# Kernel optimization log

Hardware: AMD Instinct MI355X
Metric: run time of the kernel (lower is better)

## Reference

```python
import jax, jax.numpy as jnp
import numpy as np

B, T, D_MODEL, H, W = 2, 3, 32, 256, 256
N_HEADS, N_LEVELS, N_POINTS = 4, 3, 4


def conv2d(x, w, b, padding=1, dilation=1):
    y = jax.lax.conv_general_dilated(
        x, w, window_strides=(1, 1),
        padding=[(padding, padding), (padding, padding)],
        rhs_dilation=(dilation, dilation),
        dimension_numbers=('NCHW', 'OIHW', 'NCHW'))
    return y + b[None, :, None, None]


def lrelu(x):
    return jnp.where(x >= 0, x, 0.1 * x)


def bilinear_sample(img, x, y):
    # img: (N,C,H,W); x,y: (N,H',W') pixel coords; zero padding outside (grid_sample zeros)
    N, C, Hh, Ww = img.shape
    x0 = jnp.floor(x); y0 = jnp.floor(y)
    lx = x - x0; ly = y - y0
    imf = img.reshape(N, C, Hh * Ww)
    out = jnp.zeros((N, C) + x.shape[1:], img.dtype)
    for dy, dx, wgt in ((0, 0, (1 - lx) * (1 - ly)), (0, 1, lx * (1 - ly)),
                        (1, 0, (1 - lx) * ly), (1, 1, lx * ly)):
        xi = x0 + dx; yi = y0 + dy
        valid = (xi >= 0) & (xi < Ww) & (yi >= 0) & (yi < Hh)
        idx = (jnp.clip(yi, 0, Hh - 1) * Ww + jnp.clip(xi, 0, Ww - 1)).astype(jnp.int32)
        g = jnp.take_along_axis(imf, idx.reshape(N, 1, -1), axis=2).reshape((N, C) + x.shape[1:])
        out = out + g * (wgt * valid)[:, None]
    return out


def flow_warp(x, flow):
    # torch flow_warp with align_corners=True == sampling at pixel coords grid+flow
    N, C, Hh, Ww = x.shape
    gy, gx = jnp.meshgrid(jnp.arange(Hh, dtype=x.dtype), jnp.arange(Ww, dtype=x.dtype), indexing='ij')
    return bilinear_sample(x, gx[None] + flow[:, 0], gy[None] + flow[:, 1])


def ms_deform_attn(value, sampling_locations, attention_weights, h, w):
    # value: (N, L*h*w, Hh, d); loc: (N, Lq, Hh, L, P, 2) in [0,1]; weights: (N, Lq, Hh, L, P)
    # Matches MSDA CUDA kernel: sample at loc*(W,H)-0.5, bilinear, zero pad outside.
    N, _, Hh, d = value.shape
    Lq = sampling_locations.shape[1]
    L, P = sampling_locations.shape[3], sampling_locations.shape[4]
    out = jnp.zeros((N, Lq, Hh, d), value.dtype)
    for l in range(L):
        v = value[:, l * h * w:(l + 1) * h * w].transpose(0, 2, 1, 3)  # (N,Hh,hw,d)
        loc = sampling_locations[:, :, :, l]  # (N,Lq,Hh,P,2)
        x = loc[..., 0] * w - 0.5
        y = loc[..., 1] * h - 0.5
        x0 = jnp.floor(x); y0 = jnp.floor(y)
        lx = x - x0; ly = y - y0
        samp = jnp.zeros((N, Lq, Hh, P, d), value.dtype)
        for dy, dx, wgt in ((0, 0, (1 - lx) * (1 - ly)), (0, 1, lx * (1 - ly)),
                            (1, 0, (1 - lx) * ly), (1, 1, lx * ly)):
            xi = x0 + dx; yi = y0 + dy
            valid = (xi >= 0) & (xi < w) & (yi >= 0) & (yi < h)
            idx = (jnp.clip(yi, 0, h - 1) * w + jnp.clip(xi, 0, w - 1)).astype(jnp.int32)
            idx = idx.transpose(0, 2, 1, 3).reshape(N, Hh, Lq * P)
            g = jnp.take_along_axis(v, idx[..., None], axis=2)  # (N,Hh,Lq*P,d)
            g = g.reshape(N, Hh, Lq, P, d).transpose(0, 2, 1, 3, 4)
            samp = samp + g * (wgt * valid)[..., None]
        out = out + (samp * attention_weights[:, :, :, l][..., None]).sum(axis=3)
    return out.reshape(N, Lq, Hh * d)


def setup_inputs() -> dict:
    key = jax.random.key(0)
    ks = jax.random.split(key, 24)
    def rn(k, shape, s=1.0):
        return jax.random.normal(k, shape, dtype=jnp.float32) * s
    c = D_MODEL
    nofp = N_HEADS * N_LEVELS * N_POINTS
    return {
        'frame': rn(ks[0], (B, T, c, H, W)),
        'srcframe': rn(ks[1], (B, T, c, H, W)),
        'flow_forward': rn(ks[2], (B, T - 1, 2, H, W), 2.0),
        'flow_backward': rn(ks[3], (B, T - 1, 2, H, W), 2.0),
        'W_qk': rn(ks[4], (3 * c, 3 * c + 4, 3, 3), 0.05), 'b_qk': rn(ks[5], (3 * c,), 0.05),
        'W_v': rn(ks[6], (3 * c, 3 * c, 3, 3), 0.05), 'b_v': rn(ks[7], (3 * c,), 0.05),
        'W_vp': rn(ks[8], (c, c, 3, 3), 0.05), 'b_vp': rn(ks[9], (c,), 0.05),
        'W_off': rn(ks[10], (nofp * 2, 3 * c, 3, 3), 0.01), 'b_off': rn(ks[11], (nofp * 2,), 0.5),
        'W_aw': rn(ks[12], (nofp, 3 * c, 3, 3), 0.05), 'b_aw': rn(ks[13], (nofp,), 0.05),
        'W_out': rn(ks[14], (c, c, 3, 3), 0.05), 'b_out': rn(ks[15], (c,), 0.05),
        'W_ffd': rn(ks[16], (c, c, 3, 3), 0.05), 'b_ffd': rn(ks[17], (c,), 0.05),
        'W_ff1': rn(ks[18], (c, 2 * c, 3, 3), 0.05), 'b_ff1': rn(ks[19], (c,), 0.05),
        'W_ff2': rn(ks[20], (c, c, 3, 3), 0.05), 'b_ff2': rn(ks[21], (c,), 0.05),
        'W_fu': rn(ks[22], (c, c, 1, 1), 0.05), 'b_fu': rn(ks[23], (c,), 0.05),
    }


def reference(frame, srcframe, flow_forward, flow_backward,
              W_qk, b_qk, W_v, b_v, W_vp, b_vp, W_off, b_off, W_aw, b_aw,
              W_out, b_out, W_ffd, b_ffd, W_ff1, b_ff1, W_ff2, b_ff2, W_fu, b_fu):
    b, t, c, h, w = frame.shape
    Hh, L, P = N_HEADS, N_LEVELS, N_POINTS
    d = c // Hh
    # flow-warped neighbor frames + flows -> query embedding
    warp01 = flow_warp(frame[:, 0], flow_backward[:, 0])
    warp21 = flow_warp(frame[:, 2], flow_forward[:, 1])
    qk_in = jnp.concatenate([warp01, frame[:, 1], warp21,
                             flow_forward[:, 1], flow_backward[:, 0]], axis=1)
    qureys = lrelu(conv2d(qk_in, W_qk, b_qk))                       # (b, 3c, h, w)
    value = conv2d(frame.reshape(b, t * c, h, w), W_v, b_v)         # (b, 3c, h, w)
    # --- MSDeformAttn_Fusion ---
    val = conv2d(value.reshape(b * t, c, h, w), W_vp, b_vp).reshape(b, t, c, h, w)
    off = conv2d(qureys, W_off, b_off)                               # (b, Hh*L*P*2, h, w)
    aw = conv2d(qureys, W_aw, b_aw)                                  # (b, Hh*L*P, h, w)
    value_flat = val.reshape(b, t, c, h * w).transpose(0, 1, 3, 2).reshape(b, t * h * w, Hh, d)
    off = off.reshape(b, -1, h * w).transpose(0, 2, 1).reshape(b, h * w, Hh, L, P, 2)
    aw = aw.reshape(b, -1, h * w).transpose(0, 2, 1).reshape(b, h * w, Hh, L * P)
    aw = jax.nn.softmax(aw, axis=-1).reshape(b, h * w, Hh, L, P)
    # reference points: pixel centers normalized (masks all zero -> valid_ratios == 1)
    gy, gx = jnp.meshgrid((jnp.arange(h, dtype=off.dtype) + 0.5) / h,
                          (jnp.arange(w, dtype=off.dtype) + 0.5) / w, indexing='ij')
    ref = jnp.stack([gx.reshape(-1), gy.reshape(-1)], -1)            # (hw, 2) (x, y)
    normalizer = jnp.array([w, h], dtype=off.dtype)                  # same for all levels
    loc = ref[None, :, None, None, None, :] + off / normalizer
    attn_out = ms_deform_attn(value_flat, loc, aw, h, w)             # (b, hw, c)
    out = attn_out.reshape(b, h, w, c).transpose(0, 3, 1, 2)
    out = conv2d(out, W_out, b_out)                                  # output_proj
    # --- post-attention ---
    out = conv2d(out, W_ffd, b_ffd) + frame[:, 1]
    tseq = jnp.concatenate([out, srcframe[:, 1]], axis=1)            # (b, 2c, h, w)
    ff = conv2d(lrelu(conv2d(tseq, W_ff1, b_ff1, padding=2, dilation=2)), W_ff2, b_ff2)
    out = out + ff
    out = lrelu(conv2d(out, W_fu, b_fu, padding=0))                  # fusion 1x1
    return out
```

## Files before the change

### kernel.cpp

```cpp
#include <hip/hip_runtime.h>
#include <hip/hip_bf16.h>

typedef __hip_bfloat16 bf16;
typedef unsigned short us;
typedef unsigned int u32;
typedef __attribute__((ext_vector_type(8))) short short8;
typedef __attribute__((ext_vector_type(8))) unsigned short ushortx8;
typedef __attribute__((ext_vector_type(2))) float f32x2;
typedef __attribute__((ext_vector_type(4))) float f32x4;
typedef __attribute__((ext_vector_type(16))) float f32x16;

#define HW 65536
#define IMW 256
#define IMH 256

static __device__ __forceinline__ float u2f(us u) {
  return __uint_as_float(((unsigned)u) << 16);
}
static __device__ __forceinline__ us f2bu(float x) {
  bf16 h = __float2bfloat16(x);
  return *reinterpret_cast<us*>(&h);
}
static __device__ __forceinline__ unsigned pk2(float a, float b) {
  return (unsigned)f2bu(a) | ((unsigned)f2bu(b) << 16);
}

static __device__ __forceinline__ void gload_lds16(const void* g, void* l) {
  __builtin_amdgcn_global_load_lds(
      (const __attribute__((address_space(1))) u32*)g,
      (__attribute__((address_space(3))) u32*)l, 16, 0, 0);
}

struct PrepArgs {
  const float* src[9];
  us* dst[9];
  int OC[9], CIN[9], KPAD[9], LAY[9], KCH[9];
};

__global__ __launch_bounds__(256) void prep_weights(PrepArgs a) {
  int j = blockIdx.y;
  int n = blockIdx.x * 256 + threadIdx.x;
  int OC = a.OC[j], CIN = a.CIN[j], KPAD = a.KPAD[j];
  int tot = 9 * OC * KPAD;
  if (n >= tot) return;
  int oc, k;
  if (a.LAY[j] == 0) {
    int G = OC >> 4, NKC = KPAD >> 5;
    int e = n & 7;
    int m = (n >> 3) & 15;
    int q = (n >> 7) & 3;
    int rest = n >> 9;
    int kc = rest % NKC;
    int tg = rest / NKC;
    int g = tg % G;
    int t = tg / G;
    oc = g * 16 + m;
    k = kc * 32 + q * 8 + e;
    float v = (k < CIN) ? a.src[j][(size_t)(oc * CIN + k) * 9 + t] : 0.f;
    a.dst[j][n] = f2bu(v);
  } else {
    int OCT = OC >> 5;
    int KCH = a.KCH[j];
    int KHH = KCH >> 4;
    int e = n & 7;
    int l = (n >> 3) & 63;
    int rest = n >> 9;
    int jt = rest % OCT;
    int u = rest / OCT;
    int khi = u % KHH;
    int sg = u / KHH;
    int kc = sg / 9;
    oc = jt * 32 + (l & 31);
    k = kc * KCH + khi * 16 + (l >> 5) * 8 + e;
    int t = sg - kc * 9;
    float v = (k < CIN) ? a.src[j][(size_t)(oc * CIN + k) * 9 + t] : 0.f;
    a.dst[j][n] = f2bu(v);
  }
}

__global__ __launch_bounds__(256) void frame_to_nhwc(const float* __restrict__ frame,
                                                     unsigned* __restrict__ fn) {
  int pix = blockIdx.x * 256 + threadIdx.x;
  int b = blockIdx.y;
  const float* s = frame + (size_t)b * 96 * HW + pix;
  unsigned u[48];
#pragma unroll
  for (int j = 0; j < 48; ++j)
    u[j] = pk2(s[(size_t)(2 * j) * HW], s[(size_t)(2 * j + 1) * HW]);
  unsigned* d = fn + ((size_t)b * HW + pix) * 48;
#pragma unroll
  for (int j = 0; j < 12; ++j) {
    uint4 w;
    w.x = u[4 * j]; w.y = u[4 * j + 1]; w.z = u[4 * j + 2]; w.w = u[4 * j + 3];
    *(uint4*)&d[4 * j] = w;
  }
}

static __device__ void warp_nhwc(const us* __restrict__ fn, size_t bbase, int coff,
                                 float x, float y, unsigned* uo) {
  float x0f = floorf(x), y0f = floorf(y);
  float lx = x - x0f, ly = y - y0f;
  int x0 = (int)x0f, y0 = (int)y0f;
  float wt[4] = {(1.f - lx) * (1.f - ly), lx * (1.f - ly), (1.f - lx) * ly, lx * ly};
  float acc[32] = {};
#pragma unroll
  for (int k = 0; k < 4; ++k) {
    int xi = x0 + (k & 1), yi = y0 + (k >> 1);
    if ((unsigned)xi < IMW && (unsigned)yi < IMH) {
      const ushortx8* s =
          (const ushortx8*)(fn + (bbase + (size_t)yi * IMW + xi) * 96 + coff);
      float w = wt[k];
#pragma unroll
      for (int cj = 0; cj < 4; ++cj) {
        ushortx8 vv = s[cj];
#pragma unroll
        for (int e = 0; e < 8; ++e)
          acc[cj * 8 + e] = fmaf(w, u2f(vv[e]), acc[cj * 8 + e]);
      }
    }
  }
#pragma unroll
  for (int j = 0; j < 16; ++j) uo[j] = pk2(acc[2 * j], acc[2 * j + 1]);
}

__global__ __launch_bounds__(256) void build_qkin(
    const us* __restrict__ fn, const float* __restrict__ flowf,
    const float* __restrict__ flowb, unsigned* __restrict__ qk) {
  int pix = blockIdx.x * 256 + threadIdx.x;
  int b = blockIdx.y;
  int px = pix & 255, py = pix >> 8;

  float fbx = flowb[((size_t)(b * 2 + 0) * 2 + 0) * HW + pix];
  float fby = flowb[((size_t)(b * 2 + 0) * 2 + 1) * HW + pix];
  float ffx = flowf[((size_t)(b * 2 + 1) * 2 + 0) * HW + pix];
  float ffy = flowf[((size_t)(b * 2 + 1) * 2 + 1) * HW + pix];

  unsigned u[50];
  {
    const unsigned* s = (const unsigned*)(fn + ((size_t)b * HW + pix) * 96);
#pragma unroll
    for (int j = 0; j < 16; ++j) u[16 + j] = s[16 + j];
  }
  u[48] = pk2(ffx, ffy);
  u[49] = pk2(fbx, fby);

  warp_nhwc(fn, (size_t)b * HW, 0, (float)px + fbx, (float)py + fby, &u[0]);
  warp_nhwc(fn, (size_t)b * HW, 64, (float)px + ffx, (float)py + ffy, &u[32]);

  unsigned* qb = qk + ((size_t)b * HW + pix) * 50;
#pragma unroll
  for (int j = 0; j < 25; ++j) {
    uint2 t;
    t.x = u[2 * j];
    t.y = u[2 * j + 1];
    *(uint2*)(qb + 2 * j) = t;
  }
}

template <int CIN, int CST, int KPAD, int KCH, int OCT, bool LRELU>
__global__ __launch_bounds__(256) void conv3x3_m32(
    const us* __restrict__ in, const us* __restrict__ W2,
    const float* __restrict__ bias, us* __restrict__ out, int out_cst,
    int out_coff) {
  constexpr int COLS = 34, ROWS = 10, HALO = COLS * ROWS;
  constexpr int CIPAD = KCH + 8;
  constexpr int CHc = KCH / 8;
  constexpr int KHH = KCH / 16;
  constexpr int NCH = KPAD / KCH;
  constexpr int NSTG = NCH * 9;
  constexpr int CHB = KHH * OCT;
  __shared__ alignas(16) short lds[HALO * CIPAD];
  __shared__ alignas(16) short wlds[2][CHB * 512];

  const int z = blockIdx.z;
  const int px0 = blockIdx.x * 32, py0 = blockIdx.y * 8;
  const int lane = threadIdx.x & 63;
  const int wv = threadIdx.x >> 6;
  const int n = lane & 31;
  const int sr = n >> 4;
  const int colp = n & 15;
  const int kq = lane >> 5;

  f32x16 acc[2][OCT];
#pragma unroll
  for (int f = 0; f < 2; ++f)
#pragma unroll
    for (int j = 0; j < OCT; ++j) acc[f][j] = 0.f;

  const int rb = 2 * wv + sr;
  const int base0 = ((rb + 1) * COLS + colp + 1) * CIPAD + kq * 8;
  const int base1 = base0 + 16 * CIPAD;

  int buf = 0, sg = 0;
#pragma unroll 1
  for (int kc = 0; kc < NCH; ++kc) {
    for (int c = threadIdx.x; c < HALO * CHc; c += 256) {
      int p = c / CHc, cb = c - p * CHc;
      int row = p / COLS, col = p - row * COLS;
      int gy = py0 + row - 1, gx = px0 + col - 1;
      bool ok = ((unsigned)gy < IMH) && ((unsigned)gx < IMW);
      int cil = cb * 8;
      int cig = kc * KCH + cil;
      const us* gp = in + ((size_t)z * HW + (size_t)gy * IMW + gx) * CST + cig;
      if (CIN == KPAD) {
        short8 v = (short8)0;
        if (ok) v = *(const short8*)gp;
        *(short8*)&lds[p * CIPAD + cil] = v;
      } else {
        uint2 h0; h0.x = 0; h0.y = 0;
        uint2 h1; h1.x = 0; h1.y = 0;
        if (ok && cig + 4 <= CIN) h0 = *(const uint2*)gp;
        if (ok && cig + 8 <= CIN) h1 = *(const uint2*)(gp + 4);
        *(uint2*)&lds[p * CIPAD + cil] = h0;
        *(uint2*)&lds[p * CIPAD + cil + 4] = h1;
      }
    }
    if (kc == 0) {
#pragma unroll
      for (int r = 0; r < (CHB + 3) / 4; ++r) {
        int blk = r * 4 + wv;
        if (blk < CHB)
          gload_lds16(W2 + (size_t)(blk * 64 + lane) * 8, &wlds[0][blk * 512]);
      }
    }
    __syncthreads();

#pragma unroll 1
    for (int t = 0; t < 9; ++t, ++sg) {
      if (sg + 1 < NSTG) {
        const us* wn = W2 + (size_t)(sg + 1) * (CHB * 512);
#pragma unroll
        for (int r = 0; r < (CHB + 3) / 4; ++r) {
          int blk = r * 4 + wv;
          if (blk < CHB)
            gload_lds16(wn + (size_t)(blk * 64 + lane) * 8,
                        &wlds[buf ^ 1][blk * 512]);
        }
      }
      const int dy = t / 3 - 1, dx = t - (t / 3) * 3 - 1;
      const int toff = (dy * COLS + dx) * CIPAD;
#pragma unroll
      for (int khr = 0; khr < KHH; ++khr) {
        short8 bf0 = *(const short8*)&lds[base0 + toff + khr * 16];
        short8 bf1 = *(const short8*)&lds[base1 + toff + khr * 16];
#pragma unroll
        for (int j = 0; j < OCT; ++j) {
          short8 af =
              *(const short8*)&wlds[buf][(khr * OCT + j) * 512 + lane * 8];
          acc[0][j] = __builtin_amdgcn_mfma_f32_32x32x16_bf16(af, bf0,
                                                              acc[0][j], 0, 0, 0);
          acc[1][j] = __builtin_amdgcn_mfma_f32_32x32x16_bf16(af, bf1,
                                                              acc[1][j], 0, 0, 0);
        }
      }
      __syncthreads();
      buf ^= 1;
    }
  }

  {
    int row = py0 + rb;
#pragma unroll
    for (int f = 0; f < 2; ++f) {
      int pxc = px0 + 16 * f + colp;
      us* ob =
          out + ((size_t)z * HW + (size_t)row * IMW + pxc) * out_cst + out_coff;
#pragma unroll
      for (int j = 0; j < OCT; ++j) {
#pragma unroll
        for (int hi = 0; hi < 4; ++hi) {
          int oc0 = j * 32 + hi * 8 + kq * 4;
          f32x4 bb = *(const f32x4*)&bias[oc0];
          float v0 = acc[f][j][4 * hi + 0] + bb[0];
          float v1 = acc[f][j][4 * hi + 1] + bb[1];
          float v2 = acc[f][j][4 * hi + 2] + bb[2];
          float v3 = acc[f][j][4 * hi + 3] + bb[3];
          if (LRELU) {
            v0 = v0 >= 0.f ? v0 : 0.1f * v0;
            v1 = v1 >= 0.f ? v1 : 0.1f * v1;
            v2 = v2 >= 0.f ? v2 : 0.1f * v2;
            v3 = v3 >= 0.f ? v3 : 0.1f * v3;
          }
          uint2 w;
          w.x = pk2(v0, v1);
          w.y = pk2(v2, v3);
          *(uint2*)&ob[oc0] = w;
        }
      }
    }
  }
}

template <int CIN, int CST, int KPAD, int DIL, int G, int ZDIV, int CSUB,
          int RES, int OUTMODE, bool LRELU>
__global__ __launch_bounds__(256) void conv3x3_mfma(
    const us* __restrict__ in, const us* __restrict__ W2,
    const float* __restrict__ bias, void* __restrict__ out, int out_cst,
    int out_coff, float* __restrict__ outB, const float* __restrict__ res,
    int res_cst, int res_coff) {
  constexpr int OC = G * 16;
  constexpr int COLS = 16 + 2 * DIL;
  constexpr int ROWS = 8 + 2 * DIL;
  constexpr int HALO = ROWS * COLS;
  constexpr int CIPAD = KPAD + 8;
  constexpr int CH = KPAD / 8;
  constexpr int NKC = KPAD / 32;
  constexpr int GW0 = (G + 1) / 2;
  constexpr int NU = 9 * NKC;
  __shared__ alignas(16) short lds[HALO * CIPAD];

  const int z = blockIdx.z;
  const int bin = z / ZDIV;
  const int coff = (z % ZDIV) * CSUB;
  const int px0 = blockIdx.x * 16, py0 = blockIdx.y * 8;
  const int lane = threadIdx.x & 63;
  const int wv = threadIdx.x >> 6;
  const int m = lane & 15, q = lane >> 4;
  const int gh = wv & 1, rh = wv >> 1;
  const int goff = gh * GW0;

  f32x4 acc[GW0][4];
#pragma unroll
  for (int g = 0; g < GW0; ++g)
#pragma unroll
    for (int r = 0; r < 4; ++r) acc[g][r] = 0.f;

  for (int c = threadIdx.x; c < HALO * CH; c += 256) {
    int p = c / CH, cb = c - p * CH;
    int row = p / COLS, col = p - row * COLS;
    int gy = py0 + row - DIL, gx = px0 + col - DIL;
    bool ok = ((unsigned)gy < IMH) && ((unsigned)gx < IMW);
    int ci0 = cb * 8;
    const us* gp = in + ((size_t)bin * HW + (size_t)gy * IMW + gx) * CST + coff + ci0;
    if (CIN == KPAD) {
      short8 v = (short8)0;
      if (ok) v = *(const short8*)gp;
      *(short8*)&lds[p * CIPAD + ci0] = v;
    } else {
      uint2 h0; h0.x = 0; h0.y = 0;
      uint2 h1; h1.x = 0; h1.y = 0;
      if (ok && ci0 + 4 <= CIN) h0 = *(const uint2*)gp;
      if (ok && ci0 + 8 <= CIN) h1 = *(const uint2*)(gp + 4);
      *(uint2*)&lds[p * CIPAD + ci0] = h0;
      *(uint2*)&lds[p * CIPAD + ci0 + 4] = h1;
    }
  }
  __syncthreads();

  const us* wl = W2 + (size_t)lane * 8;
  short8 af[2][GW0];
#pragma unroll
  for (int g = 0; g < GW0; ++g)
    if (goff + g < G)
      af[0][g] = *(const short8*)(wl + (size_t)((goff + g) * NKC) * 512);

#pragma unroll
  for (int u = 0; u < NU; ++u) {
    const int t = u / NKC, kc = u - t * NKC;
    if (u + 1 < NU) {
      const int t1 = (u + 1) / NKC, kc1 = (u + 1) - t1 * NKC;
#pragma unroll
      for (int g = 0; g < GW0; ++g)
        if (goff + g < G)
          af[(u + 1) & 1][g] =
              *(const short8*)(wl + (size_t)((t1 * G + goff + g) * NKC + kc1) * 512);
    }
    const int dy = t / 3 - 1, dx = t - (t / 3) * 3 - 1;
    short8 bfr[4];
#pragma unroll
    for (int r = 0; r < 4; ++r) {
      int rr = rh * 4 + r + DIL + dy * DIL;
      int cc = m + DIL + dx * DIL;
      bfr[r] = *(const short8*)&lds[(rr * COLS + cc) * CIPAD + kc * 32 + q * 8];
    }
#pragma unroll
    for (int g = 0; g < GW0; ++g)
      if (goff + g < G)
#pragma unroll
        for (int r = 0; r < 4; ++r)
          acc[g][r] = __builtin_amdgcn_mfma_f32_16x16x32_bf16(af[u & 1][g], bfr[r],
                                                              acc[g][r], 0, 0, 0);
  }

#pragma unroll
  for (int g = 0; g < GW0; ++g) {
    if (goff + g < G) {
      int oc0 = (goff + g) * 16 + q * 4;
      f32x4 bb = *(const f32x4*)&bias[oc0];
#pragma unroll
      for (int r = 0; r < 4; ++r) {
        int py = py0 + rh * 4 + r;
        int px = px0 + m;
        size_t pix = (size_t)py * IMW + px;
        f32x4 v;
#pragma unroll
        for (int e = 0; e < 4; ++e) {
          float x = acc[g][r][e] + bb[e];
          if (LRELU) x = x >= 0.f ? x : 0.1f * x;
          v[e] = x;
        }
        if (RES == 1) {
          f32x4 rv = *(const f32x4*)&res[((size_t)z * HW + pix) * res_cst + oc0];
#pragma unroll
          for (int e = 0; e < 4; ++e) v[e] += rv[e];
        }
        if (RES == 2) {
#pragma unroll
          for (int e = 0; e < 4; ++e)
            v[e] += res[((size_t)z * res_cst + res_coff + oc0 + e) * HW + pix];
        }
        if (OUTMODE == 0 || OUTMODE == 3) {
          uint2 w;
          w.x = pk2(v[0], v[1]);
          w.y = pk2(v[2], v[3]);
          *(uint2*)&((us*)out)[((size_t)z * HW + pix) * out_cst + out_coff + oc0] = w;
        }
        if (OUTMODE == 2)
          *(f32x4*)&((float*)out)[((size_t)z * HW + pix) * out_cst + oc0] = v;
        if (OUTMODE == 3)
          *(f32x4*)&outB[((size_t)z * HW + pix) * 32 + oc0] = v;
      }
    }
  }
}

__global__ __launch_bounds__(256) void deform_attn(
    const us* __restrict__ valp, const us* __restrict__ off,
    const float* __restrict__ aw, us* __restrict__ outp) {
  int tid = threadIdx.x;
  int half = tid & 1;
  int hh = (tid >> 1) & 3;
  int pix = blockIdx.x * 32 + (tid >> 3);
  int b = blockIdx.y;
  int px = pix & (IMW - 1), py = pix >> 8;

  us os[12];
  {
    const uint2* ob = (const uint2*)(off + ((size_t)b * HW + pix) * 96 +
                                     hh * 24 + half * 12);
    uint2 a0 = ob[0], a1 = ob[1], a2 = ob[2];
    *(uint2*)&os[0] = a0;
    *(uint2*)&os[4] = a1;
    *(uint2*)&os[8] = a2;
  }
  float wv[6];
  {
    const f32x2* ab = (const f32x2*)(aw + ((size_t)b * HW + pix) * 48 +
                                     hh * 12 + half * 6);
    f32x2 a0 = ab[0], a1 = ab[1], a2 = ab[2];
    wv[0] = a0.x; wv[1] = a0.y; wv[2] = a1.x;
    wv[3] = a1.y; wv[4] = a2.x; wv[5] = a2.y;
  }

  float m6 = wv[0];
#pragma unroll
  for (int i = 1; i < 6; ++i) m6 = fmaxf(m6, wv[i]);
  float mx = fmaxf(m6, __shfl_xor(m6, 1));
  float s6 = 0.f;
#pragma unroll
  for (int i = 0; i < 6; ++i) {
    wv[i] = __expf(wv[i] - mx);
    s6 += wv[i];
  }
  float inv = 1.f / (s6 + __shfl_xor(s6, 1));

  f32x2 acc2[4];
#pragma unroll
  for (int j = 0; j < 4; ++j) acc2[j] = 0.f;

#pragma unroll
  for (int i = 0; i < 6; ++i) {
    int pp = half * 6 + i;
    int l = pp >> 2;
    const us* vbase = valp + ((size_t)(b * 3 + l) * HW) * 32 + hh * 8;
    float x = (float)px + u2f(os[2 * i]);
    float y = (float)py + u2f(os[2 * i + 1]);
    float x0f = floorf(x), y0f = floorf(y);
    float lx = x - x0f, ly = y - y0f;
    int x0 = (int)x0f, y0 = (int)y0f;
    bool vx0 = (unsigned)x0 < IMW, vx1 = (unsigned)(x0 + 1) < IMW;
    bool vy0 = (unsigned)y0 < IMH, vy1 = (unsigned)(y0 + 1) < IMH;
    float a = wv[i] * inv;
    float ax0 = (1.f - lx) * a, ax1 = lx * a;
    float w00 = ax0 * (1.f - ly), w01 = ax1 * (1.f - ly);
    float w10 = ax0 * ly, w11 = ax1 * ly;
    const us* p00 = vbase + (size_t)((long)(y0 * IMW + x0)) * 32;
#pragma unroll
    for (int c = 0; c < 4; ++c) {
      bool ok = (c & 1 ? vx1 : vx0) && (c & 2 ? vy1 : vy0);
      float w = (c == 0) ? w00 : (c == 1) ? w01 : (c == 2) ? w10 : w11;
      const us* p = p00 + (c & 1) * 32 + (c >> 1) * (IMW * 32);
      if (ok) {
        uint4 uu = *(const uint4*)p;
        unsigned uarr[4] = {uu.x, uu.y, uu.z, uu.w};
#pragma unroll
        for (int j = 0; j < 4; ++j) {
          f32x2 v;
          v.x = __uint_as_float(uarr[j] << 16);
          v.y = __uint_as_float(uarr[j] & 0xffff0000u);
          acc2[j] += v * w;
        }
      }
    }
  }

  float accf[8];
#pragma unroll
  for (int j = 0; j < 4; ++j) {
    accf[2 * j] = acc2[j].x + __shfl_xor(acc2[j].x, 1);
    accf[2 * j + 1] = acc2[j].y + __shfl_xor(acc2[j].y, 1);
  }
  if (half == 0) {
    ushortx8 sv;
#pragma unroll
    for (int dd = 0; dd < 8; ++dd) sv[dd] = f2bu(accf[dd]);
    *(ushortx8*)(outp + ((size_t)b * HW + pix) * 32 + hh * 8) = sv;
  }
}

__global__ __launch_bounds__(256) void copy_src(const float* __restrict__ src,
                                                unsigned* __restrict__ out1b) {
  int pix = blockIdx.x * 256 + threadIdx.x;
  int b = blockIdx.y;
  const float* s = src + ((size_t)(b * 3 + 1) * 32) * HW + pix;
  unsigned u[16];
#pragma unroll
  for (int j = 0; j < 16; ++j)
    u[j] = pk2(s[(size_t)(2 * j) * HW], s[(size_t)(2 * j + 1) * HW]);
  unsigned* d = out1b + ((size_t)b * HW + pix) * 32 + 16;
#pragma unroll
  for (int j = 0; j < 4; ++j) {
    uint4 w;
    w.x = u[4 * j]; w.y = u[4 * j + 1]; w.z = u[4 * j + 2]; w.w = u[4 * j + 3];
    *(uint4*)&d[4 * j] = w;
  }
}

__global__ __launch_bounds__(256) void conv1x1_fu(
    const float* __restrict__ in, const float* __restrict__ wgt,
    const float* __restrict__ bias, float* __restrict__ out) {
  int pix = blockIdx.x * 256 + threadIdx.x;
  int b = blockIdx.y;
  float vin[32];
  {
    const f32x4* s = (const f32x4*)(in + ((size_t)b * HW + pix) * 32);
#pragma unroll
    for (int j = 0; j < 8; ++j) {
      f32x4 v = s[j];
#pragma unroll
      for (int e = 0; e < 4; ++e) vin[4 * j + e] = v[e];
    }
  }
#pragma unroll 1
  for (int oc = 0; oc < 32; ++oc) {
    float a = bias[oc];
#pragma unroll
    for (int ci = 0; ci < 32; ++ci) a = fmaf(wgt[oc * 32 + ci], vin[ci], a);
    a = a >= 0.f ? a : 0.1f * a;
    out[((size_t)b * 32 + oc) * HW + pix] = a;
  }
}

extern "C" void kernel_launch(void* const* d_in, const int* in_sizes, int n_in,
                              void* d_out, int out_size, void* d_ws, size_t ws_size,
                              hipStream_t stream) {
  (void)in_sizes; (void)n_in; (void)out_size;
  if (ws_size < 25614592ull * 4) return;

  const float* frame = (const float*)d_in[0];
  const float* srcframe = (const float*)d_in[1];
  const float* flowf = (const float*)d_in[2];
  const float* flowb = (const float*)d_in[3];

  float* ws = (float*)d_ws;
  us* wsu = (us*)d_ws;

  static const int w2off[9] = {0,      110592, 193536, 202752, 285696,
                               327168, 336384, 345600, 364032};
  us* fnhwc = (us*)(ws + 186624);
  unsigned* qk_u = (unsigned*)(ws + 6478080);
  us* qk = (us*)qk_u;
  us* Q = (us*)(ws + 13031680);
  us* V = (us*)(ws + 6478080);
  us* Vp = (us*)(ws + 19323136);
  us* offb = (us*)(ws + 186624);
  float* awb = (float*)(ws + 6478080);
  us* attn = (us*)(ws + 13031680);
  us* convout = (us*)(ws + 13031680 + 2097152);
  us* out1b = (us*)(ws + 6478080);
  unsigned* out1b_u = (unsigned*)out1b;
  float* out1f = (float*)(ws + 19323136);
  us* ff1out = (us*)(ws + 186624);
  float* out2 = (float*)(ws + 13031680);

  {
    PrepArgs pa;
    static const int srcidx[9] = {4, 6, 8, 10, 12, 14, 16, 18, 20};
    static const int OCs[9] = {96, 96, 32, 96, 48, 32, 32, 32, 32};
    static const int CINs[9] = {100, 96, 32, 96, 96, 32, 32, 64, 32};
    static const int KPADs[9] = {128, 96, 32, 96, 96, 32, 32, 64, 32};
    static const int LAYs[9] = {1, 1, 0, 1, 0, 0, 0, 0, 0};
    static const int KCHs[9] = {32, 32, 32, 32, 32, 32, 32, 32, 32};
    for (int i = 0; i < 9; ++i) {
      pa.src[i] = (const float*)d_in[srcidx[i]];
      pa.dst[i] = wsu + w2off[i];
      pa.OC[i] = OCs[i];
      pa.CIN[i] = CINs[i];
      pa.KPAD[i] = KPADs[i];
      pa.LAY[i] = LAYs[i];
      pa.KCH[i] = KCHs[i];
    }
    prep_weights<<<dim3(432, 9), 256, 0, stream>>>(pa);
  }

  frame_to_nhwc<<<dim3(256, 2), 256, 0, stream>>>(frame, (unsigned*)fnhwc);

  build_qkin<<<dim3(256, 2), 256, 0, stream>>>(fnhwc, flowf, flowb, qk_u);

  dim3 cg2(16, 32, 2);
  dim3 cg32(8, 32, 2);

  conv3x3_m32<100, 100, 128, 32, 3, true><<<cg32, 256, 0, stream>>>(
      qk, wsu + w2off[0], (const float*)d_in[5], Q, 96, 0);

  conv3x3_m32<96, 96, 96, 32, 3, false><<<cg32, 256, 0, stream>>>(
      fnhwc, wsu + w2off[1], (const float*)d_in[7], V, 96, 0);

  conv3x3_mfma<32, 96, 32, 1, 2, 3, 32, 0, 0, false><<<dim3(16, 32, 6), 256, 0, stream>>>(
      V, wsu + w2off[2], (const float*)d_in[9], Vp, 32, 0, nullptr, nullptr, 0, 0);

  conv3x3_m32<96, 96, 96, 32, 3, false><<<cg32, 256, 0, stream>>>(
      Q, wsu + w2off[3], (const float*)d_in[11], offb, 96, 0);

  conv3x3_mfma<96, 96, 96, 1, 3, 1, 0, 0, 2, false><<<cg2, 256, 0, stream>>>(
      Q, wsu + w2off[4], (const float*)d_in[13], awb, 48, 0, nullptr, nullptr, 0, 0);

  deform_attn<<<dim3(2048, 2), 256, 0, stream>>>(Vp, offb, awb, attn);

  conv3x3_mfma<32, 32, 32, 1, 2, 1, 0, 0, 0, false><<<cg2, 256, 0, stream>>>(
      attn, wsu + w2off[5], (const float*)d_in[15], convout, 32, 0, nullptr, nullptr, 0, 0);

  conv3x3_mfma<32, 32, 32, 1, 2, 1, 0, 2, 3, false><<<cg2, 256, 0, stream>>>(
      convout, wsu + w2off[6], (const float*)d_in[17], out1b, 64, 0, out1f, frame, 96, 32);

  copy_src<<<dim3(256, 2), 256, 0, stream>>>(srcframe, out1b_u);

  conv3x3_mfma<64, 64, 64, 2, 2, 1, 0, 0, 0, true><<<cg2, 256, 0, stream>>>(
      out1b, wsu + w2off[7], (const float*)d_in[19], ff1out, 32, 0, nullptr, nullptr, 0, 0);

  conv3x3_mfma<32, 32, 32, 1, 2, 1, 0, 1, 2, false><<<cg2, 256, 0, stream>>>(
      ff1out, wsu + w2off[8], (const float*)d_in[21], out2, 32, 0, nullptr, out1f, 32, 0);

  conv1x1_fu<<<dim3(256, 2), 256, 0, stream>>>(out2, (const float*)d_in[22],
                                               (const float*)d_in[23], (float*)d_out);
}
```

Before: 460.5 us.

## Load conv weights directly into registers with double buffering instead of LDS

Weight fragments for each 3x3 tap are now read from global memory straight into a two-slot register array and prefetched one tap ahead. This replaces the LDS weight staging done with global_load_lds, and the tap loop is fully unrolled. The aim is to drop the per-tap __syncthreads and the LDS weight traffic. In exchange every wave loads the same weights from global/L2 on its own, and the register footprint grows, which risks occupancy loss or spills.

```diff
diff --git a/kernel.cpp b/kernel.cpp
--- a/kernel.cpp
+++ b/kernel.cpp
@@ -23,12 +23,6 @@
 }
 static __device__ __forceinline__ unsigned pk2(float a, float b) {
   return (unsigned)f2bu(a) | ((unsigned)f2bu(b) << 16);
-}
-
-static __device__ __forceinline__ void gload_lds16(const void* g, void* l) {
-  __builtin_amdgcn_global_load_lds(
-      (const __attribute__((address_space(1))) u32*)g,
-      (__attribute__((address_space(3))) u32*)l, 16, 0, 0);
 }
 
 struct PrepArgs {
@@ -167,10 +161,8 @@
   constexpr int CHc = KCH / 8;
   constexpr int KHH = KCH / 16;
   constexpr int NCH = KPAD / KCH;
-  constexpr int NSTG = NCH * 9;
-  constexpr int CHB = KHH * OCT;
+  constexpr int WST = KHH * OCT * 512;
   __shared__ alignas(16) short lds[HALO * CIPAD];
-  __shared__ alignas(16) short wlds[2][CHB * 512];
 
   const int z = blockIdx.z;
   const int px0 = blockIdx.x * 32, py0 = blockIdx.y * 8;
@@ -191,9 +183,12 @@
   const int base0 = ((rb + 1) * COLS + colp + 1) * CIPAD + kq * 8;
   const int base1 = base0 + 16 * CIPAD;
 
-  int buf = 0, sg = 0;
+  const us* wl = W2 + (size_t)lane * 8;
+  short8 af[2][KHH][OCT];
+
 #pragma unroll 1
   for (int kc = 0; kc < NCH; ++kc) {
+    if (kc) __syncthreads();
     for (int c = threadIdx.x; c < HALO * CHc; c += 256) {
       int p = c / CHc, cb = c - p * CHc;
       int row = p / COLS, col = p - row * COLS;
@@ -215,27 +210,26 @@
         *(uint2*)&lds[p * CIPAD + cil + 4] = h1;
       }
     }
-    if (kc == 0) {
-#pragma unroll
-      for (int r = 0; r < (CHB + 3) / 4; ++r) {
-        int blk = r * 4 + wv;
-        if (blk < CHB)
-          gload_lds16(W2 + (size_t)(blk * 64 + lane) * 8, &wlds[0][blk * 512]);
-      }
+    {
+      const us* w0 = wl + (size_t)(kc * 9) * WST;
+#pragma unroll
+      for (int khi = 0; khi < KHH; ++khi)
+#pragma unroll
+        for (int j = 0; j < OCT; ++j)
+          af[0][khi][j] = *(const short8*)(w0 + (khi * OCT + j) * 512);
     }
     __syncthreads();
 
-#pragma unroll 1
-    for (int t = 0; t < 9; ++t, ++sg) {
-      if (sg + 1 < NSTG) {
-        const us* wn = W2 + (size_t)(sg + 1) * (CHB * 512);
-#pragma unroll
-        for (int r = 0; r < (CHB + 3) / 4; ++r) {
-          int blk = r * 4 + wv;
-          if (blk < CHB)
-            gload_lds16(wn + (size_t)(blk * 64 + lane) * 8,
-                        &wlds[buf ^ 1][blk * 512]);
-        }
+#pragma unroll
+    for (int t = 0; t < 9; ++t) {
+      if (t < 8) {
+        const us* wn = wl + (size_t)(kc * 9 + t + 1) * WST;
+#pragma unroll
+        for (int khi = 0; khi < KHH; ++khi)
+#pragma unroll
+          for (int j = 0; j < OCT; ++j)
+            af[(t + 1) & 1][khi][j] =
+                *(const short8*)(wn + (khi * OCT + j) * 512);
       }
       const int dy = t / 3 - 1, dx = t - (t / 3) * 3 - 1;
       const int toff = (dy * COLS + dx) * CIPAD;
@@ -245,16 +239,12 @@
         short8 bf1 = *(const short8*)&lds[base1 + toff + khr * 16];
 #pragma unroll
         for (int j = 0; j < OCT; ++j) {
-          short8 af =
-              *(const short8*)&wlds[buf][(khr * OCT + j) * 512 + lane * 8];
-          acc[0][j] = __builtin_amdgcn_mfma_f32_32x32x16_bf16(af, bf0,
-                                                              acc[0][j], 0, 0, 0);
-          acc[1][j] = __builtin_amdgcn_mfma_f32_32x32x16_bf16(af, bf1,
-                                                              acc[1][j], 0, 0, 0);
+          acc[0][j] = __builtin_amdgcn_mfma_f32_32x32x16_bf16(
+              af[t & 1][khr][j], bf0, acc[0][j], 0, 0, 0);
+          acc[1][j] = __builtin_amdgcn_mfma_f32_32x32x16_bf16(
+              af[t & 1][khr][j], bf1, acc[1][j], 0, 0, 0);
         }
       }
-      __syncthreads();
-      buf ^= 1;
     }
   }
 
```

New measurement: 470.4 us. 1.02x slower.
